# Optimization experiments

Measured on AMD Instinct MI355X. Metric: run time of the kernel, lower is better.

## Reference

```python
import jax, jax.numpy as jnp
import numpy as np
from jax import lax

H = 64          # num_heads
P = 64          # head_dim
N = 128         # ssm_state_size
G = 8           # n_groups
K = 4           # conv_kernel
D_MODEL = 4096  # hidden_size
I = H * P                      # intermediate_size = 4096
GN = G * N                     # groups_time_state_size = 1024
CONV_DIM = I + 2 * GN          # 6144
PROJ = I + CONV_DIM + H        # 10304
EPS = 1e-5
GROUP_SIZE = I // G            # 512


def setup_inputs() -> dict:
    key = jax.random.key(0)
    ks = jax.random.split(key, 6)
    B, L = 2, 2048
    s = 0.02
    return {
        "hidden_states": jax.random.normal(ks[0], (B, L, D_MODEL), jnp.float32),
        "in_proj_w": jax.random.normal(ks[1], (PROJ, D_MODEL), jnp.float32) * s,
        "conv_weight": jax.random.normal(ks[2], (CONV_DIM, K), jnp.float32) * s,
        "conv_bias": jnp.zeros((CONV_DIM,), jnp.float32),
        "dt_bias": jnp.ones((H,), jnp.float32),
        "A_log": jnp.log(jnp.arange(1, H + 1, dtype=jnp.float32)),
        "D": jnp.ones((H,), jnp.float32),
        "norm_weight": jnp.ones((I,), jnp.float32),
        "out_proj_w": jax.random.normal(ks[3], (D_MODEL, I), jnp.float32) * s,
    }


def reference(hidden_states, in_proj_w, conv_weight, conv_bias, dt_bias, A_log, D, norm_weight, out_proj_w):
    B, L, _ = hidden_states.shape

    # in_proj, then split into gate / conv-stream / dt
    proj = jnp.einsum("bld,pd->blp", hidden_states, in_proj_w)
    gate = proj[..., :I]
    hbc = proj[..., I:I + CONV_DIM]          # (B, L, conv_dim), pre-conv
    dt = proj[..., -H:]                       # (B, L, H)

    # depthwise causal conv1d + SiLU
    pad = jnp.pad(hbc, ((0, 0), (K - 1, 0), (0, 0)))
    conv = conv_bias
    for k in range(K):  # K=4, tiny fixed loop
        conv = conv + pad[:, k:k + L, :] * conv_weight[:, k]
    xBC = jax.nn.silu(conv)

    x = xBC[..., :I].reshape(B, L, H, P)                        # (B,L,H,P)
    Bm = xBC[..., I:I + GN].reshape(B, L, G, N)
    Cm = xBC[..., I + GN:].reshape(B, L, G, N)
    hpg = H // G
    B_h = jnp.repeat(Bm, hpg, axis=2)                            # (B,L,H,N)
    C_h = jnp.repeat(Cm, hpg, axis=2)                            # (B,L,H,N)

    # dt processing: softplus(dt + dt_bias), limits (0, inf)
    dt_p = jax.nn.softplus(dt + dt_bias)                         # (B,L,H)
    A = -jnp.exp(A_log)                                          # (H,)
    dA = jnp.exp(dt_p * A)                                       # (B,L,H)
    dtx = dt_p[..., None] * x                                    # (B,L,H,P)

    # selective scan over sequence (O(L)), state: (B,H,P,N)
    def step(state, inp):
        dA_t, dtx_t, B_t, C_t = inp
        state = state * dA_t[..., None, None] + dtx_t[..., None] * B_t[:, :, None, :]
        y_t = jnp.einsum("bhpn,bhn->bhp", state, C_t)
        return state, y_t

    xs = (jnp.moveaxis(dA, 1, 0), jnp.moveaxis(dtx, 1, 0),
          jnp.moveaxis(B_h, 1, 0), jnp.moveaxis(C_h, 1, 0))
    state0 = jnp.zeros((B, H, P, N), jnp.float32)
    final_state, ys = lax.scan(step, state0, xs)
    y = jnp.moveaxis(ys, 0, 1) + x * D[None, None, :, None]      # (B,L,H,P)
    y = y.reshape(B, L, I)

    # gated grouped RMSNorm: 8 independent RMSNorms over 512 elems each
    yg = y.reshape(B, L, G, GROUP_SIZE)
    var = jnp.mean(yg * yg, axis=-1, keepdims=True)
    yn = (yg * lax.rsqrt(var + EPS)).reshape(B, L, I) * norm_weight
    yn = yn * jax.nn.silu(gate)

    out = jnp.einsum("bli,di->bld", yn, out_proj_w)

    conv_state_new = jnp.moveaxis(hbc[:, L - (K - 1):, :], 1, 2)  # (B, conv_dim, K-1)
    return out, conv_state_new, final_state
```

## Files before the change

kernel.cpp:

```cpp
#include <hip/hip_runtime.h>
#include <cstdint>
#include <cstddef>

typedef __bf16 bf16;
typedef float f32x4 __attribute__((ext_vector_type(4)));
typedef bf16 bf16x8 __attribute__((ext_vector_type(8)));
typedef bf16 bf16x4 __attribute__((ext_vector_type(4)));

#define DM    4096
#define LL    2048
#define BB    2
#define BT    4096
#define II    4096
#define GN_   1024
#define CONVD 6144
#define PROJD 10304
#define NPAD  10496
#define HH    64
#define PP    64
#define NN    128
#define CT    64
#define NC    32

#define OUT_OFS_CONV  16777216
#define OUT_OFS_STATE 16814080

#define WS_HSB    0UL
#define WS_WINB   33554432UL
#define WS_DSB    0UL
#define WS_PROJ   119537664UL
#define WS_XBC    291504128UL
#define WS_DTDA   392167424UL
#define WS_Y      394264576UL
#define WS_WOUTB  0UL
#define WS_YNB    33554432UL

__device__ __forceinline__ void gl2lds16(const void* g, void* l) {
  __builtin_amdgcn_global_load_lds(
      (__attribute__((address_space(1))) unsigned int*)(uintptr_t)g,
      (__attribute__((address_space(3))) unsigned int*)(uintptr_t)l, 16, 0, 0);
}

__global__ __launch_bounds__(256) void cast_kernel(const float* __restrict__ src,
                                                   bf16* __restrict__ dst,
                                                   long nsrc, long ndst) {
  long i = ((long)blockIdx.x * 256 + threadIdx.x) * 4;
  if (i >= ndst) return;
  bf16x4 o;
  if (i < nsrc) {
    float4 v = *(const float4*)(src + i);
    o[0] = (bf16)v.x; o[1] = (bf16)v.y; o[2] = (bf16)v.z; o[3] = (bf16)v.w;
  } else {
    o[0] = (bf16)0.f; o[1] = (bf16)0.f; o[2] = (bf16)0.f; o[3] = (bf16)0.f;
  }
  *(bf16x4*)(dst + i) = o;
}

#define BARF() do { asm volatile("" ::: "memory");                    \
                    __builtin_amdgcn_s_barrier();                     \
                    asm volatile("" ::: "memory"); } while (0)
#define WAITLGKM0() do { asm volatile("s_waitcnt lgkmcnt(0)" ::: "memory"); \
                         __builtin_amdgcn_sched_barrier(0); } while (0)
#define WAITVM(n) asm volatile("s_waitcnt vmcnt(" #n ")" ::: "memory")
#define PRIO1 __builtin_amdgcn_s_setprio(1)
#define PRIO0 __builtin_amdgcn_s_setprio(0)

__device__ __forceinline__ void stage_A_half(const bf16* __restrict__ A, int K,
                                             int arow, int kt, bf16* lds,
                                             int h, int tid) {
#pragma unroll
  for (int j = 0; j < 2; ++j) {
    const int r  = h * 64 + j * 128 + (tid >> 3);
    const int cb = (tid & 7) * 16;
    const int cs = cb ^ ((r & 7) << 4);
    gl2lds16(A + (size_t)(arow + r) * K + kt * 64 + (cs >> 1),
             lds + r * 64 + (cb >> 1));
  }
}
__device__ __forceinline__ void stage_B_half(const bf16* __restrict__ B, int K,
                                             int brow, int kt, bf16* lds,
                                             int h, int tid) {
#pragma unroll
  for (int j = 0; j < 2; ++j) {
    const int quarter = j * 2 + (tid >> 8);
    const int kq = tid & 255;
    const int r  = quarter * 64 + h * 32 + (kq >> 3);
    const int cb = (kq & 7) * 16;
    const int cs = cb ^ ((r & 7) << 4);
    gl2lds16(B + (size_t)(brow + r) * K + kt * 64 + (cs >> 1),
             lds + r * 64 + (cb >> 1));
  }
}

#define LDA4(p, mh) do {                                                     \
  _Pragma("unroll") for (int mt = 0; mt < 4; ++mt)                           \
  _Pragma("unroll") for (int kk = 0; kk < 2; ++kk) {                         \
    const int rr = wm * 128 + (mh) * 64 + mt * 16 + l16;                     \
    const int cc = (kk * 64 + quad * 16) ^ ((rr & 7) << 4);                  \
    a_[mt][kk] = *(const bf16x8*)((const char*)(&sA[p][rr][0]) + cc);        \
  } } while (0)

#define LDB2(p, np, barr) do {                                               \
  _Pragma("unroll") for (int nt = 0; nt < 2; ++nt)                           \
  _Pragma("unroll") for (int kk = 0; kk < 2; ++kk) {                         \
    const int rr = wn * 64 + (np) * 32 + nt * 16 + l16;                      \
    const int cc = (kk * 64 + quad * 16) ^ ((rr & 7) << 4);                  \
    barr[nt][kk] = *(const bf16x8*)((const char*)(&sB[p][rr][0]) + cc);      \
  } } while (0)

#define MFMAQ(mh, barr, nb0) do {                                            \
  _Pragma("unroll") for (int kk = 0; kk < 2; ++kk)                           \
  _Pragma("unroll") for (int mt = 0; mt < 4; ++mt)                           \
  _Pragma("unroll") for (int nt = 0; nt < 2; ++nt)                           \
    acc[(mh) * 4 + mt][(nb0) + nt] = __builtin_amdgcn_mfma_f32_16x16x32_bf16(\
        a_[mt][kk], barr[nt][kk], acc[(mh) * 4 + mt][(nb0) + nt], 0, 0, 0);  \
  } while (0)

__global__ __launch_bounds__(512, 2) void gemm256(const bf16* __restrict__ A,
                                                  const bf16* __restrict__ B,
                                                  float* __restrict__ C,
                                                  int M, int N, int K, int NB) {
  __shared__ __align__(16) bf16 sA[2][256][64];
  __shared__ __align__(16) bf16 sB[2][256][64];

  const int tid  = threadIdx.x;
  const int wave = tid >> 6, lane = tid & 63;
  const int l16  = lane & 15, quad = lane >> 4;
  const int wm   = wave >> 2, wn = wave & 3;

  const int nwg = gridDim.x;
  const int q = nwg >> 3, r8 = nwg & 7;
  const int xcd = blockIdx.x & 7, idx = blockIdx.x >> 3;
  const int wgid = (xcd < r8 ? xcd * (q + 1) : r8 * (q + 1) + (xcd - r8) * q) + idx;
  const int mb = wgid / NB, nb = wgid - mb * NB;
  const int arow = mb * 256, brow = nb * 256;

  f32x4 acc[8][4];
#pragma unroll
  for (int i = 0; i < 8; ++i)
#pragma unroll
    for (int j = 0; j < 4; ++j) acc[i][j] = (f32x4)0.f;

  const int NT = K >> 6;

  stage_A_half(A, K, arow, 0, &sA[0][0][0], 0, tid);
  stage_B_half(B, K, brow, 0, &sB[0][0][0], 0, tid);
  stage_A_half(A, K, arow, 0, &sA[0][0][0], 1, tid);
  stage_B_half(B, K, brow, 0, &sB[0][0][0], 1, tid);
  stage_A_half(A, K, arow, 1, &sA[1][0][0], 0, tid);
  stage_B_half(B, K, brow, 1, &sB[1][0][0], 0, tid);
  stage_A_half(A, K, arow, 1, &sA[1][0][0], 1, tid);
  WAITVM(6);
  BARF();

  bf16x8 a_[4][2], b0_[2][2], b1_[2][2];

  for (int i = 0; i < NT / 2; ++i) {
    const int t1o = 2 * i + 1;
    const int t2  = (2 * i + 2 < NT) ? 2 * i + 2 : NT - 1;
    const int t3  = (2 * i + 3 < NT) ? 2 * i + 3 : NT - 1;

    LDA4(0, 0); LDB2(0, 0, b0_);
    stage_B_half(B, K, brow, t1o, &sB[1][0][0], 1, tid);
    BARF(); WAITLGKM0();
    PRIO1; MFMAQ(0, b0_, 0); PRIO0;
    BARF();
    LDB2(0, 1, b1_);
    stage_A_half(A, K, arow, t2, &sA[0][0][0], 0, tid);
    BARF(); WAITLGKM0();
    PRIO1; MFMAQ(0, b1_, 2); PRIO0;
    BARF();
    LDA4(0, 1);
    stage_B_half(B, K, brow, t2, &sB[0][0][0], 0, tid);
    BARF(); WAITLGKM0();
    PRIO1; MFMAQ(1, b1_, 2); PRIO0;
    BARF();
    stage_A_half(A, K, arow, t2, &sA[0][0][0], 1, tid);
    WAITVM(6);
    BARF();
    PRIO1; MFMAQ(1, b0_, 0); PRIO0;
    BARF();
    LDA4(1, 0); LDB2(1, 0, b0_);
    stage_B_half(B, K, brow, t2, &sB[0][0][0], 1, tid);
    BARF(); WAITLGKM0();
    PRIO1; MFMAQ(0, b0_, 0); PRIO0;
    BARF();
    LDB2(1, 1, b1_);
    stage_A_half(A, K, arow, t3, &sA[1][0][0], 0, tid);
    BARF(); WAITLGKM0();
    PRIO1; MFMAQ(0, b1_, 2); PRIO0;
    BARF();
    LDA4(1, 1);
    stage_B_half(B, K, brow, t3, &sB[1][0][0], 0, tid);
    BARF(); WAITLGKM0();
    PRIO1; MFMAQ(1, b1_, 2); PRIO0;
    BARF();
    stage_A_half(A, K, arow, t3, &sA[1][0][0], 1, tid);
    WAITVM(6);
    BARF();
    PRIO1; MFMAQ(1, b0_, 0); PRIO0;
    BARF();
  }
  asm volatile("s_waitcnt vmcnt(0)" ::: "memory");
  __builtin_amdgcn_s_barrier();

#pragma unroll
  for (int mt = 0; mt < 8; ++mt) {
    const int row0 = arow + wm * 128 + mt * 16 + quad * 4;
#pragma unroll
    for (int nt = 0; nt < 4; ++nt) {
      const int col = brow + wn * 64 + nt * 16 + l16;
#pragma unroll
      for (int r = 0; r < 4; ++r)
        C[(size_t)(row0 + r) * N + col] = acc[mt][nt][r];
    }
  }
}

__global__ __launch_bounds__(256) void conv_kernel(const float* __restrict__ proj,
                                                   const float* __restrict__ cw,
                                                   const float* __restrict__ cb,
                                                   float* __restrict__ xbc) {
  const int c  = blockIdx.x * 256 + threadIdx.x;
  const int bt = blockIdx.y;
  const int t  = bt & (LL - 1);
  const float4 w = *(const float4*)(cw + c * 4);
  const float* p = proj + (size_t)bt * NPAD + II + c;
  float acc = cb[c];
  if (t >= 3) {
    acc += p[-3 * (ptrdiff_t)NPAD] * w.x + p[-2 * (ptrdiff_t)NPAD] * w.y
         + p[-(ptrdiff_t)NPAD] * w.z + p[0] * w.w;
  } else {
    const float* pw = &w.x;
    for (int k = 3 - t; k <= 3; ++k)
      acc += p[(ptrdiff_t)(k - 3) * NPAD] * pw[k];
  }
  xbc[(size_t)bt * CONVD + c] = acc / (1.f + __expf(-acc));
}

__global__ __launch_bounds__(256) void dt_kernel(const float* __restrict__ proj,
                                                 const float* __restrict__ dt_bias,
                                                 const float* __restrict__ A_log,
                                                 float* __restrict__ dtda) {
  const int idx = blockIdx.x * 256 + threadIdx.x;
  const int bt = idx >> 6, h = idx & 63;
  const float z = proj[(size_t)bt * NPAD + (II + CONVD) + h] + dt_bias[h];
  const float sp = (z > 20.f) ? z : log1pf(__expf(z));
  const float a = -__expf(A_log[h]);
  float2 o; o.x = sp; o.y = __expf(sp * a);
  *(float2*)(dtda + (size_t)idx * 2) = o;
}

__global__ __launch_bounds__(256) void convstate_kernel(const float* __restrict__ proj,
                                                        float* __restrict__ outp) {
  const int idx = blockIdx.x * 256 + threadIdx.x;
  if (idx >= BB * CONVD * 3) return;
  const int b = idx / (CONVD * 3);
  const int r = idx - b * CONVD * 3;
  const int c = r / 3, j = r - c * 3;
  outp[idx] = proj[((size_t)b * LL + (LL - 3 + j)) * NPAD + II + c];
}

__global__ __launch_bounds__(256) void chunkA_kernel(const float* __restrict__ xbc,
                                                     const float* __restrict__ dtda,
                                                     const float* __restrict__ A_log,
                                                     float* __restrict__ ybuf,
                                                     bf16* __restrict__ dsb) {
  const int h = blockIdx.x, c = blockIdx.y, b = blockIdx.z;
  const int g = h >> 3;
  const int tid = threadIdx.x;
  const int wave = tid >> 6, lane = tid & 63;
  const int l16 = lane & 15, quad = lane >> 4;

  __shared__ __align__(16) bf16 CsBt[8192];
  __shared__ __align__(16) bf16 Bs[64][128];
  __shared__ __align__(16) bf16 Xt[64][64];
  __shared__ __align__(16) bf16 Ws[64][64];
  __shared__ float cums[64], dtps[64], wls[64];

  bf16 (*Cs)[128] = (bf16(*)[128])CsBt;
  bf16 (*Bt)[64]  = (bf16(*)[64])CsBt;

  const size_t rowbase = ((size_t)b * LL + (size_t)c * CT) * CONVD;

  {
    const int i = tid >> 2, col0 = (tid & 3) * 32;
    const float* gpC = xbc + rowbase + (size_t)i * CONVD + (II + GN_) + g * 128 + col0;
    const float* gpB = xbc + rowbase + (size_t)i * CONVD + II + g * 128 + col0;
    const int sx = i & 15;
#pragma unroll
    for (int k = 0; k < 8; ++k) {
      const int n = col0 + k * 4;
      const int eo = (((n >> 3) ^ sx) * 8) + (n & 7);
      float4 v = *(const float4*)(gpC + k * 4);
      bf16x4 o; o[0]=(bf16)v.x; o[1]=(bf16)v.y; o[2]=(bf16)v.z; o[3]=(bf16)v.w;
      *(bf16x4*)(&Cs[i][0] + eo) = o;
      float4 u = *(const float4*)(gpB + k * 4);
      bf16x4 p; p[0]=(bf16)u.x; p[1]=(bf16)u.y; p[2]=(bf16)u.z; p[3]=(bf16)u.w;
      *(bf16x4*)(&Bs[i][0] + eo) = p;
    }
  }
  {
    const int j = tid >> 2, p0 = (tid & 3) * 16;
    const float* gpX = xbc + rowbase + (size_t)j * CONVD + h * 64 + p0;
#pragma unroll
    for (int k = 0; k < 4; ++k) {
      float4 v = *(const float4*)(gpX + k * 4);
      const float* vv = (const float*)&v;
#pragma unroll
      for (int e = 0; e < 4; ++e) {
        const int pp = p0 + k * 4 + e;
        Xt[pp][(((j >> 3) ^ (pp & 7)) * 8) + (j & 7)] = (bf16)vv[e];
      }
    }
  }
  if (wave == 0) {
    const float Ah = -__expf(A_log[h]);
    float2 dd = *(const float2*)(dtda + ((size_t)((b * LL + c * CT + lane)) * 64 + h) * 2);
    float s = dd.x * Ah;
#pragma unroll
    for (int d = 1; d < 64; d <<= 1) {
      float v = __shfl_up(s, d);
      if (lane >= d) s += v;
    }
    const float tot = __shfl(s, 63);
    cums[lane] = s;
    dtps[lane] = dd.x;
    wls[lane]  = __expf(tot - s) * dd.x;
  }
  __syncthreads();

  const int mrow = wave * 16 + l16;
  {
    f32x4 accg[4];
#pragma unroll
    for (int nt = 0; nt < 4; ++nt) accg[nt] = (f32x4)0.f;
#pragma unroll
    for (int k0 = 0; k0 < 128; k0 += 32) {
      bf16x8 af = *(const bf16x8*)&Cs[mrow][(((k0 >> 3) + quad) ^ (mrow & 15)) * 8];
#pragma unroll
      for (int nt = 0; nt < 4; ++nt) {
        const int nrow = nt * 16 + l16;
        bf16x8 bfr = *(const bf16x8*)&Bs[nrow][(((k0 >> 3) + quad) ^ (nrow & 15)) * 8];
        accg[nt] = __builtin_amdgcn_mfma_f32_16x16x32_bf16(af, bfr, accg[nt], 0, 0, 0);
      }
    }
#pragma unroll
    for (int nt = 0; nt < 4; ++nt) {
      const int j = nt * 16 + l16;
#pragma unroll
      for (int r = 0; r < 4; ++r) {
        const int i = wave * 16 + quad * 4 + r;
        float v = 0.f;
        if (j <= i) v = accg[nt][r] * __expf(cums[i] - cums[j]) * dtps[j];
        Ws[i][(((j >> 3) ^ (i & 7)) * 8) + (j & 7)] = (bf16)v;
      }
    }
  }
  __syncthreads();

  {
    const int n = tid >> 1, j0 = (tid & 1) * 32;
#pragma unroll
    for (int jj = 0; jj < 32; ++jj) {
      const int j = j0 + jj;
      bf16 v = Bs[j][(((n >> 3) ^ (j & 15)) * 8) + (n & 7)];
      Bt[n][(((j >> 3) ^ (n & 7)) * 8) + (j & 7)] = v;
    }
  }
  __syncthreads();

  f32x4 accy[4];
#pragma unroll
  for (int pt = 0; pt < 4; ++pt) accy[pt] = (f32x4)0.f;
#pragma unroll
  for (int k0 = 0; k0 < 64; k0 += 32) {
    bf16x8 af = *(const bf16x8*)&Ws[mrow][(((k0 >> 3) + quad) ^ (mrow & 7)) * 8];
#pragma unroll
    for (int pt = 0; pt < 4; ++pt) {
      const int prow = pt * 16 + l16;
      bf16x8 bfr = *(const bf16x8*)&Xt[prow][(((k0 >> 3) + quad) ^ (prow & 7)) * 8];
      accy[pt] = __builtin_amdgcn_mfma_f32_16x16x32_bf16(af, bfr, accy[pt], 0, 0, 0);
    }
  }

  f32x4 accs[8];
#pragma unroll
  for (int nt = 0; nt < 8; ++nt) accs[nt] = (f32x4)0.f;
#pragma unroll
  for (int k0 = 0; k0 < 64; k0 += 32) {
    bf16x8 axr = *(const bf16x8*)&Xt[mrow][(((k0 >> 3) + quad) ^ (mrow & 7)) * 8];
    bf16x8 ax;
#pragma unroll
    for (int e = 0; e < 8; ++e)
      ax[e] = (bf16)((float)axr[e] * wls[k0 + quad * 8 + e]);
#pragma unroll
    for (int nt = 0; nt < 8; ++nt) {
      const int nrow = nt * 16 + l16;
      bf16x8 bfr = *(const bf16x8*)&Bt[nrow][(((k0 >> 3) + quad) ^ (nrow & 7)) * 8];
      accs[nt] = __builtin_amdgcn_mfma_f32_16x16x32_bf16(ax, bfr, accs[nt], 0, 0, 0);
    }
  }

#pragma unroll
  for (int pt = 0; pt < 4; ++pt) {
#pragma unroll
    for (int r = 0; r < 4; ++r) {
      const int i = wave * 16 + quad * 4 + r;
      ybuf[((size_t)(b * LL + c * CT + i)) * II + h * 64 + pt * 16 + l16] = accy[pt][r];
    }
  }
  const size_t dbase = (((size_t)(b * HH + h)) * NC + c) * (CT * NN);
#pragma unroll
  for (int nt = 0; nt < 8; ++nt) {
#pragma unroll
    for (int r = 0; r < 4; ++r) {
      const int p = wave * 16 + quad * 4 + r;
      dsb[dbase + (size_t)p * NN + nt * 16 + l16] = (bf16)accs[nt][r];
    }
  }
}

__global__ __launch_bounds__(256) void chain_kernel(const float* __restrict__ dtda,
                                                    const float* __restrict__ A_log,
                                                    bf16* __restrict__ dsb,
                                                    float* __restrict__ fst) {
  const int blk = blockIdx.x;
  const int b = blk >> 7, h = (blk >> 1) & 63, half = blk & 1;
  const int tid = threadIdx.x, wave = tid >> 6, lane = tid & 63;
  __shared__ float DcL[NC];

  const float Ah = -__expf(A_log[h]);
#pragma unroll
  for (int cc = 0; cc < 8; ++cc) {
    const int c = wave * 8 + cc;
    float2 dd = *(const float2*)(dtda + ((size_t)(b * LL + c * CT + lane) * 64 + h) * 2);
    float a = dd.x * Ah;
#pragma unroll
    for (int m = 1; m <= 32; m <<= 1) a += __shfl_xor(a, m);
    if (lane == 0) DcL[c] = __expf(a);
  }
  __syncthreads();

  const int local = half * 4096 + tid * 16;
  const size_t base = ((size_t)(b * HH + h)) * NC * (CT * NN) + local;
  float s[16];
#pragma unroll
  for (int e = 0; e < 16; ++e) s[e] = 0.f;

  for (int c = 0; c < NC; ++c) {
    bf16* p = dsb + base + (size_t)c * (CT * NN);
    bf16x8 d0 = *(const bf16x8*)(p);
    bf16x8 d1 = *(const bf16x8*)(p + 8);
    const float dc = DcL[c];
    bf16x8 o0, o1;
#pragma unroll
    for (int e = 0; e < 8; ++e) { o0[e] = (bf16)s[e]; o1[e] = (bf16)s[8 + e]; }
    *(bf16x8*)(p)     = o0;
    *(bf16x8*)(p + 8) = o1;
#pragma unroll
    for (int e = 0; e < 8; ++e) {
      s[e]     = s[e] * dc + (float)d0[e];
      s[8 + e] = s[8 + e] * dc + (float)d1[e];
    }
  }
  float* fp = fst + ((size_t)(b * HH + h)) * (PP * NN) + local;
#pragma unroll
  for (int k = 0; k < 4; ++k) {
    float4 v = { s[k * 4], s[k * 4 + 1], s[k * 4 + 2], s[k * 4 + 3] };
    *(float4*)(fp + k * 4) = v;
  }
}

__global__ __launch_bounds__(256) void chunkB_kernel(const float* __restrict__ xbc,
                                                     const float* __restrict__ dtda,
                                                     const float* __restrict__ A_log,
                                                     const float* __restrict__ Dv,
                                                     const bf16* __restrict__ spb,
                                                     float* __restrict__ ybuf) {
  const int h = blockIdx.x, c = blockIdx.y, b = blockIdx.z;
  const int g = h >> 3;
  const int tid = threadIdx.x;
  const int wave = tid >> 6, lane = tid & 63;
  const int l16 = lane & 15, quad = lane >> 4;

  __shared__ __align__(16) bf16 Cs[64][128];
  __shared__ __align__(16) bf16 Sp[64][128];
  __shared__ float es[64];

  const size_t rowbase = ((size_t)b * LL + (size_t)c * CT) * CONVD;
  {
    const int i = tid >> 2, col0 = (tid & 3) * 32;
    const float* gpC = xbc + rowbase + (size_t)i * CONVD + (II + GN_) + g * 128 + col0;
    const int sx = i & 15;
#pragma unroll
    for (int k = 0; k < 8; ++k) {
      const int n = col0 + k * 4;
      float4 v = *(const float4*)(gpC + k * 4);
      bf16x4 o; o[0]=(bf16)v.x; o[1]=(bf16)v.y; o[2]=(bf16)v.z; o[3]=(bf16)v.w;
      *(bf16x4*)(&Cs[i][0] + (((n >> 3) ^ sx) * 8) + (n & 7)) = o;
    }
  }
  {
    const int p = tid >> 2, nseg = (tid & 3) * 32;
    const bf16* gp = spb + (((size_t)(b * HH + h)) * NC + c) * (CT * NN) + (size_t)p * NN + nseg;
    const int sx = p & 15;
#pragma unroll
    for (int k = 0; k < 4; ++k) {
      const int n0 = nseg + k * 8;
      bf16x8 v = *(const bf16x8*)(gp + k * 8);
      *(bf16x8*)(&Sp[p][0] + (((n0 >> 3) ^ sx) * 8)) = v;
    }
  }
  if (wave == 0) {
    const float Ah = -__expf(A_log[h]);
    float2 dd = *(const float2*)(dtda + ((size_t)(b * LL + c * CT + lane) * 64 + h) * 2);
    float s = dd.x * Ah;
#pragma unroll
    for (int d = 1; d < 64; d <<= 1) {
      float v = __shfl_up(s, d);
      if (lane >= d) s += v;
    }
    es[lane] = __expf(s);
  }
  __syncthreads();

  const int mrow = wave * 16 + l16;
  f32x4 acc[4];
#pragma unroll
  for (int pt = 0; pt < 4; ++pt) acc[pt] = (f32x4)0.f;
#pragma unroll
  for (int k0 = 0; k0 < 128; k0 += 32) {
    bf16x8 af = *(const bf16x8*)&Cs[mrow][(((k0 >> 3) + quad) ^ (mrow & 15)) * 8];
#pragma unroll
    for (int pt = 0; pt < 4; ++pt) {
      const int prow = pt * 16 + l16;
      bf16x8 bfr = *(const bf16x8*)&Sp[prow][(((k0 >> 3) + quad) ^ (prow & 15)) * 8];
      acc[pt] = __builtin_amdgcn_mfma_f32_16x16x32_bf16(af, bfr, acc[pt], 0, 0, 0);
    }
  }

  const float Dh = Dv[h];
#pragma unroll
  for (int pt = 0; pt < 4; ++pt) {
#pragma unroll
    for (int r = 0; r < 4; ++r) {
      const int i = wave * 16 + quad * 4 + r;
      const int p = pt * 16 + l16;
      const size_t row = (size_t)(b * LL + c * CT + i);
      const size_t ya = row * II + h * 64 + p;
      const float xv = xbc[row * CONVD + h * 64 + p];
      ybuf[ya] = acc[pt][r] * es[i] + ybuf[ya] + Dh * xv;
    }
  }
}

__global__ __launch_bounds__(256) void norm_kernel(const float* __restrict__ y,
                                                   const float* __restrict__ proj,
                                                   const float* __restrict__ nw,
                                                   bf16* __restrict__ yn) {
  const int bt = blockIdx.x, tid = threadIdx.x;
  const float* yr = y + (size_t)bt * II + tid * 16;
  float4 v[4];
  float ss = 0.f;
#pragma unroll
  for (int i = 0; i < 4; ++i) {
    v[i] = *(const float4*)(yr + i * 4);
    ss += v[i].x * v[i].x + v[i].y * v[i].y + v[i].z * v[i].z + v[i].w * v[i].w;
  }
#pragma unroll
  for (int m = 1; m <= 16; m <<= 1) ss += __shfl_xor(ss, m);
  const float rstd = rsqrtf(ss * (1.f / 512.f) + 1e-5f);

  const float* gr  = proj + (size_t)bt * NPAD + tid * 16;
  const float* nwr = nw + tid * 16;
  bf16x8 o0, o1;
#pragma unroll
  for (int i = 0; i < 4; ++i) {
    float4 gv = *(const float4*)(gr + i * 4);
    float4 nv = *(const float4*)(nwr + i * 4);
    const float* vv = (const float*)&v[i];
    const float* gg = (const float*)&gv;
    const float* nn = (const float*)&nv;
#pragma unroll
    for (int j = 0; j < 4; ++j) {
      const float gate = gg[j];
      const float val = vv[j] * rstd * nn[j] * (gate / (1.f + __expf(-gate)));
      if (i < 2) o0[i * 4 + j] = (bf16)val;
      else       o1[(i - 2) * 4 + j] = (bf16)val;
    }
  }
  bf16* dst = yn + (size_t)bt * II + tid * 16;
  *(bf16x8*)(dst)     = o0;
  *(bf16x8*)(dst + 8) = o1;
}

extern "C" void kernel_launch(void* const* d_in, const int* in_sizes, int n_in,
                              void* d_out, int out_size, void* d_ws, size_t ws_size,
                              hipStream_t stream) {
  const float* hs      = (const float*)d_in[0];
  const float* w_in    = (const float*)d_in[1];
  const float* cw      = (const float*)d_in[2];
  const float* cb      = (const float*)d_in[3];
  const float* dt_bias = (const float*)d_in[4];
  const float* A_log   = (const float*)d_in[5];
  const float* Dv      = (const float*)d_in[6];
  const float* nw      = (const float*)d_in[7];
  const float* w_out   = (const float*)d_in[8];

  char* ws = (char*)d_ws;
  bf16*  hsb   = (bf16*)(ws + WS_HSB);
  bf16*  winb  = (bf16*)(ws + WS_WINB);
  bf16*  dsb   = (bf16*)(ws + WS_DSB);
  float* proj  = (float*)(ws + WS_PROJ);
  float* xbc   = (float*)(ws + WS_XBC);
  float* dtda  = (float*)(ws + WS_DTDA);
  float* ybuf  = (float*)(ws + WS_Y);
  bf16*  ynb   = (bf16*)(ws + WS_YNB);
  bf16*  woutb = (bf16*)(ws + WS_WOUTB);

  float* outp = (float*)d_out;

  cast_kernel<<<16384, 256, 0, stream>>>(hs, hsb, 16777216L, 16777216L);
  cast_kernel<<<41984, 256, 0, stream>>>(w_in, winb, (long)PROJD * DM, (long)NPAD * DM);

  gemm256<<<(BT / 256) * (NPAD / 256), 512, 0, stream>>>(hsb, winb, proj, BT, NPAD, DM, NPAD / 256);

  conv_kernel<<<dim3(CONVD / 256, BT), 256, 0, stream>>>(proj, cw, cb, xbc);
  dt_kernel<<<(BT * HH) / 256, 256, 0, stream>>>(proj, dt_bias, A_log, dtda);
  convstate_kernel<<<(BB * CONVD * 3 + 255) / 256, 256, 0, stream>>>(proj, outp + OUT_OFS_CONV);

  chunkA_kernel<<<dim3(HH, NC, BB), 256, 0, stream>>>(xbc, dtda, A_log, ybuf, dsb);
  chain_kernel<<<BB * HH * 2, 256, 0, stream>>>(dtda, A_log, dsb, outp + OUT_OFS_STATE);
  chunkB_kernel<<<dim3(HH, NC, BB), 256, 0, stream>>>(xbc, dtda, A_log, Dv, dsb, ybuf);

  cast_kernel<<<16384, 256, 0, stream>>>(w_out, woutb, 16777216L, 16777216L);
  norm_kernel<<<BT, 256, 0, stream>>>(ybuf, proj, nw, ynb);

  gemm256<<<(BT / 256) * (DM / 256), 512, 0, stream>>>(ynb, woutb, outp, BT, DM, II, DM / 256);
}
```

Before: 1.091 ms.

## Store conv output in bf16, tile conv over time, split chain kernel finer

The conv kernel now processes 64 timesteps per thread with a sliding register window, cutting the redundant reads of neighbouring rows. It writes the SiLU output as bf16 instead of fp32, which halves conv-output traffic and lets chunkA and chunkB load it directly with vector loads instead of casting per element. The chain kernel is split into quarters rather than halves to run more blocks. Rounding to bf16 earlier also makes the D*x skip term less precise.

Result: faster. 974.2 us (-10.7%).

```diff
diff --git a/kernel.cpp b/kernel.cpp
--- a/kernel.cpp
+++ b/kernel.cpp
@@ -217,25 +217,33 @@
   }
 }
 
+#define CTILE 64
 __global__ __launch_bounds__(256) void conv_kernel(const float* __restrict__ proj,
                                                    const float* __restrict__ cw,
                                                    const float* __restrict__ cb,
-                                                   float* __restrict__ xbc) {
-  const int c  = blockIdx.x * 256 + threadIdx.x;
-  const int bt = blockIdx.y;
-  const int t  = bt & (LL - 1);
+                                                   bf16* __restrict__ xbc) {
+  const int c   = blockIdx.x * 256 + threadIdx.x;
+  const int bt0 = blockIdx.y * CTILE;
+  const int t0  = bt0 & (LL - 1);
   const float4 w = *(const float4*)(cw + c * 4);
-  const float* p = proj + (size_t)bt * NPAD + II + c;
-  float acc = cb[c];
-  if (t >= 3) {
-    acc += p[-3 * (ptrdiff_t)NPAD] * w.x + p[-2 * (ptrdiff_t)NPAD] * w.y
-         + p[-(ptrdiff_t)NPAD] * w.z + p[0] * w.w;
+  const float bias = cb[c];
+  const float* p = proj + (size_t)bt0 * NPAD + II + c;
+  float h0, h1, h2;
+  if (t0 == 0) {
+    h0 = 0.f; h1 = 0.f; h2 = 0.f;
   } else {
-    const float* pw = &w.x;
-    for (int k = 3 - t; k <= 3; ++k)
-      acc += p[(ptrdiff_t)(k - 3) * NPAD] * pw[k];
-  }
-  xbc[(size_t)bt * CONVD + c] = acc / (1.f + __expf(-acc));
+    h0 = p[-3 * (ptrdiff_t)NPAD];
+    h1 = p[-2 * (ptrdiff_t)NPAD];
+    h2 = p[-(ptrdiff_t)NPAD];
+  }
+  bf16* q = xbc + (size_t)bt0 * CONVD + c;
+#pragma unroll 8
+  for (int t = 0; t < CTILE; ++t) {
+    const float cur = p[(ptrdiff_t)t * NPAD];
+    const float acc = bias + h0 * w.x + h1 * w.y + h2 * w.z + cur * w.w;
+    q[(size_t)t * CONVD] = (bf16)(acc / (1.f + __expf(-acc)));
+    h0 = h1; h1 = h2; h2 = cur;
+  }
 }
 
 __global__ __launch_bounds__(256) void dt_kernel(const float* __restrict__ proj,
@@ -261,7 +269,7 @@
   outp[idx] = proj[((size_t)b * LL + (LL - 3 + j)) * NPAD + II + c];
 }
 
-__global__ __launch_bounds__(256) void chunkA_kernel(const float* __restrict__ xbc,
+__global__ __launch_bounds__(256) void chunkA_kernel(const bf16* __restrict__ xbc,
                                                      const float* __restrict__ dtda,
                                                      const float* __restrict__ A_log,
                                                      float* __restrict__ ybuf,
@@ -285,32 +293,27 @@
 
   {
     const int i = tid >> 2, col0 = (tid & 3) * 32;
-    const float* gpC = xbc + rowbase + (size_t)i * CONVD + (II + GN_) + g * 128 + col0;
-    const float* gpB = xbc + rowbase + (size_t)i * CONVD + II + g * 128 + col0;
+    const bf16* gpC = xbc + rowbase + (size_t)i * CONVD + (II + GN_) + g * 128 + col0;
+    const bf16* gpB = xbc + rowbase + (size_t)i * CONVD + II + g * 128 + col0;
     const int sx = i & 15;
 #pragma unroll
-    for (int k = 0; k < 8; ++k) {
-      const int n = col0 + k * 4;
-      const int eo = (((n >> 3) ^ sx) * 8) + (n & 7);
-      float4 v = *(const float4*)(gpC + k * 4);
-      bf16x4 o; o[0]=(bf16)v.x; o[1]=(bf16)v.y; o[2]=(bf16)v.z; o[3]=(bf16)v.w;
-      *(bf16x4*)(&Cs[i][0] + eo) = o;
-      float4 u = *(const float4*)(gpB + k * 4);
-      bf16x4 p; p[0]=(bf16)u.x; p[1]=(bf16)u.y; p[2]=(bf16)u.z; p[3]=(bf16)u.w;
-      *(bf16x4*)(&Bs[i][0] + eo) = p;
+    for (int k = 0; k < 4; ++k) {
+      const int n0 = col0 + k * 8;
+      const int eo = ((n0 >> 3) ^ sx) * 8;
+      *(bf16x8*)(&Cs[i][0] + eo) = *(const bf16x8*)(gpC + k * 8);
+      *(bf16x8*)(&Bs[i][0] + eo) = *(const bf16x8*)(gpB + k * 8);
     }
   }
   {
     const int j = tid >> 2, p0 = (tid & 3) * 16;
-    const float* gpX = xbc + rowbase + (size_t)j * CONVD + h * 64 + p0;
-#pragma unroll
-    for (int k = 0; k < 4; ++k) {
-      float4 v = *(const float4*)(gpX + k * 4);
-      const float* vv = (const float*)&v;
-#pragma unroll
-      for (int e = 0; e < 4; ++e) {
-        const int pp = p0 + k * 4 + e;
-        Xt[pp][(((j >> 3) ^ (pp & 7)) * 8) + (j & 7)] = (bf16)vv[e];
+    const bf16* gpX = xbc + rowbase + (size_t)j * CONVD + h * 64 + p0;
+#pragma unroll
+    for (int k = 0; k < 2; ++k) {
+      bf16x8 v = *(const bf16x8*)(gpX + k * 8);
+#pragma unroll
+      for (int e = 0; e < 8; ++e) {
+        const int pp = p0 + k * 8 + e;
+        Xt[pp][(((j >> 3) ^ (pp & 7)) * 8) + (j & 7)] = v[e];
       }
     }
   }
@@ -426,7 +429,7 @@
                                                     bf16* __restrict__ dsb,
                                                     float* __restrict__ fst) {
   const int blk = blockIdx.x;
-  const int b = blk >> 7, h = (blk >> 1) & 63, half = blk & 1;
+  const int b = blk >> 8, h = (blk >> 2) & 63, qtr = blk & 3;
   const int tid = threadIdx.x, wave = tid >> 6, lane = tid & 63;
   __shared__ float DcL[NC];
 
@@ -442,37 +445,32 @@
   }
   __syncthreads();
 
-  const int local = half * 4096 + tid * 16;
+  const int local = qtr * 2048 + tid * 8;
   const size_t base = ((size_t)(b * HH + h)) * NC * (CT * NN) + local;
-  float s[16];
-#pragma unroll
-  for (int e = 0; e < 16; ++e) s[e] = 0.f;
+  float s[8];
+#pragma unroll
+  for (int e = 0; e < 8; ++e) s[e] = 0.f;
 
   for (int c = 0; c < NC; ++c) {
     bf16* p = dsb + base + (size_t)c * (CT * NN);
     bf16x8 d0 = *(const bf16x8*)(p);
-    bf16x8 d1 = *(const bf16x8*)(p + 8);
     const float dc = DcL[c];
-    bf16x8 o0, o1;
-#pragma unroll
-    for (int e = 0; e < 8; ++e) { o0[e] = (bf16)s[e]; o1[e] = (bf16)s[8 + e]; }
-    *(bf16x8*)(p)     = o0;
-    *(bf16x8*)(p + 8) = o1;
-#pragma unroll
-    for (int e = 0; e < 8; ++e) {
-      s[e]     = s[e] * dc + (float)d0[e];
-      s[8 + e] = s[8 + e] * dc + (float)d1[e];
-    }
+    bf16x8 o0;
+#pragma unroll
+    for (int e = 0; e < 8; ++e) o0[e] = (bf16)s[e];
+    *(bf16x8*)(p) = o0;
+#pragma unroll
+    for (int e = 0; e < 8; ++e) s[e] = s[e] * dc + (float)d0[e];
   }
   float* fp = fst + ((size_t)(b * HH + h)) * (PP * NN) + local;
 #pragma unroll
-  for (int k = 0; k < 4; ++k) {
+  for (int k = 0; k < 2; ++k) {
     float4 v = { s[k * 4], s[k * 4 + 1], s[k * 4 + 2], s[k * 4 + 3] };
     *(float4*)(fp + k * 4) = v;
   }
 }
 
-__global__ __launch_bounds__(256) void chunkB_kernel(const float* __restrict__ xbc,
+__global__ __launch_bounds__(256) void chunkB_kernel(const bf16* __restrict__ xbc,
                                                      const float* __restrict__ dtda,
                                                      const float* __restrict__ A_log,
                                                      const float* __restrict__ Dv,
@@ -491,14 +489,12 @@
   const size_t rowbase = ((size_t)b * LL + (size_t)c * CT) * CONVD;
   {
     const int i = tid >> 2, col0 = (tid & 3) * 32;
-    const float* gpC = xbc + rowbase + (size_t)i * CONVD + (II + GN_) + g * 128 + col0;
+    const bf16* gpC = xbc + rowbase + (size_t)i * CONVD + (II + GN_) + g * 128 + col0;
     const int sx = i & 15;
 #pragma unroll
-    for (int k = 0; k < 8; ++k) {
-      const int n = col0 + k * 4;
-      float4 v = *(const float4*)(gpC + k * 4);
-      bf16x4 o; o[0]=(bf16)v.x; o[1]=(bf16)v.y; o[2]=(bf16)v.z; o[3]=(bf16)v.w;
-      *(bf16x4*)(&Cs[i][0] + (((n >> 3) ^ sx) * 8) + (n & 7)) = o;
+    for (int k = 0; k < 4; ++k) {
+      const int n0 = col0 + k * 8;
+      *(bf16x8*)(&Cs[i][0] + (((n0 >> 3) ^ sx) * 8)) = *(const bf16x8*)(gpC + k * 8);
     }
   }
   {
@@ -549,7 +545,7 @@
       const int p = pt * 16 + l16;
       const size_t row = (size_t)(b * LL + c * CT + i);
       const size_t ya = row * II + h * 64 + p;
-      const float xv = xbc[row * CONVD + h * 64 + p];
+      const float xv = (float)xbc[row * CONVD + h * 64 + p];
       ybuf[ya] = acc[pt][r] * es[i] + ybuf[ya] + Dh * xv;
     }
   }
@@ -613,7 +609,7 @@
   bf16*  winb  = (bf16*)(ws + WS_WINB);
   bf16*  dsb   = (bf16*)(ws + WS_DSB);
   float* proj  = (float*)(ws + WS_PROJ);
-  float* xbc   = (float*)(ws + WS_XBC);
+  bf16*  xbc   = (bf16*)(ws + WS_XBC);
   float* dtda  = (float*)(ws + WS_DTDA);
   float* ybuf  = (float*)(ws + WS_Y);
   bf16*  ynb   = (bf16*)(ws + WS_YNB);
@@ -626,12 +622,12 @@
 
   gemm256<<<(BT / 256) * (NPAD / 256), 512, 0, stream>>>(hsb, winb, proj, BT, NPAD, DM, NPAD / 256);
 
-  conv_kernel<<<dim3(CONVD / 256, BT), 256, 0, stream>>>(proj, cw, cb, xbc);
+  conv_kernel<<<dim3(CONVD / 256, BT / CTILE), 256, 0, stream>>>(proj, cw, cb, xbc);
   dt_kernel<<<(BT * HH) / 256, 256, 0, stream>>>(proj, dt_bias, A_log, dtda);
   convstate_kernel<<<(BB * CONVD * 3 + 255) / 256, 256, 0, stream>>>(proj, outp + OUT_OFS_CONV);
 
   chunkA_kernel<<<dim3(HH, NC, BB), 256, 0, stream>>>(xbc, dtda, A_log, ybuf, dsb);
-  chain_kernel<<<BB * HH * 2, 256, 0, stream>>>(dtda, A_log, dsb, outp + OUT_OFS_STATE);
+  chain_kernel<<<BB * HH * 4, 256, 0, stream>>>(dtda, A_log, dsb, outp + OUT_OFS_STATE);
   chunkB_kernel<<<dim3(HH, NC, BB), 256, 0, stream>>>(xbc, dtda, A_log, Dv, dsb, ybuf);
 
   cast_kernel<<<16384, 256, 0, stream>>>(w_out, woutb, 16777216L, 16777216L);
```
